# Kernel optimization log

Measured on AMD Instinct MI355X. Metric: run time of the kernel, lower is better.

Reference implementation:

```python
import jax, jax.numpy as jnp
import numpy as np

N_USERS = 100000
N_ITEMS = 50000
D = 64
E = 3200000
N_LAYERS = 2
ALPHA = 0.1


def setup_inputs() -> dict:
    key = jax.random.key(0)
    k1, k2, k3, k4 = jax.random.split(key, 4)
    user_emb0 = jax.random.normal(k1, (N_USERS, D), jnp.float32) * 0.01
    item_emb0 = jax.random.normal(k2, (N_ITEMS, D), jnp.float32) * 0.01
    edge_u = jax.random.randint(k3, (E,), 0, N_USERS, dtype=jnp.int32)
    edge_i = jax.random.randint(k4, (E,), 0, N_ITEMS, dtype=jnp.int32)
    ones = jnp.ones((E,), jnp.float32)
    # row-normalization exactly as the torch module: A_ui = D_u^{-1} R, A_iu = D_i^{-1} R^T
    deg_u = jax.ops.segment_sum(ones, edge_u, num_segments=N_USERS)
    deg_i = jax.ops.segment_sum(ones, edge_i, num_segments=N_ITEMS)
    deg_u = jnp.where(deg_u == 0, 1.0, deg_u)
    deg_i = jnp.where(deg_i == 0, 1.0, deg_i)
    a_ui_vals = 1.0 / deg_u[edge_u]  # value of A_ui at (u, i)
    a_iu_vals = 1.0 / deg_i[edge_i]  # value of A_iu at (i, u)
    return {
        "user_emb0": user_emb0,
        "item_emb0": item_emb0,
        "a_ui_vals": a_ui_vals,
        "a_iu_vals": a_iu_vals,
        "edge_u": edge_u,
        "edge_i": edge_i,
    }


def _spmm(vals, dst_idx, src_idx, src_emb, n_dst):
    # out[dst] = sum_e vals[e] * src_emb[src_idx[e]]  -- gather, scale, scatter-add
    gathered = src_emb[src_idx] * vals[:, None]  # [E, D]
    return jax.ops.segment_sum(gathered, dst_idx, num_segments=n_dst)


def reference(user_emb0, item_emb0, a_ui_vals, a_iu_vals, edge_u, edge_i):
    user_layers = [user_emb0]
    item_layers = [item_emb0]
    for _ in range(N_LAYERS):
        u_new = _spmm(a_ui_vals, edge_u, edge_i, item_layers[-1], N_USERS) + ALPHA * user_emb0
        i_new = _spmm(a_iu_vals, edge_i, edge_u, user_layers[-1], N_ITEMS) + ALPHA * item_emb0
        user_layers.append(u_new)
        item_layers.append(i_new)
    # [n_layers+1, N_USERS, D], [n_layers+1, N_ITEMS, D]
    return jnp.stack(user_layers, 0), jnp.stack(item_layers, 0)
```

## Files before the change

### kernel.cpp

```cpp
#include <hip/hip_runtime.h>


constexpr int N_USERS = 100000;
constexpr int N_ITEMS = 50000;
constexpr int N_ROWS  = N_USERS + N_ITEMS;
constexpr int D = 64;
constexpr int E_EDGES = 3200000;
constexpr float ALPHA = 0.1f;

constexpr long long NUF = (long long)N_USERS * D;
constexpr long long NIF = (long long)N_ITEMS * D;

constexpr int SB_SHIFT = 8;
constexpr int SB_ROWS  = 1 << SB_SHIFT;
constexpr int NSB      = (N_ROWS + SB_ROWS - 1) >> SB_SHIFT;
constexpr int CAP      = 20480;

constexpr int P1_EDGES   = 8192;
constexpr int P1_THREADS = 512;
constexpr int P1_EPT     = P1_EDGES / P1_THREADS;
constexpr int P2_THREADS = 512;

__global__ void init_layer0(const float* __restrict__ uemb,
                            const float* __restrict__ iemb,
                            float* __restrict__ out) {
    long long idx = (long long)blockIdx.x * blockDim.x + threadIdx.x;
    if (idx < NUF) out[idx] = uemb[idx];
    if (idx < NIF) out[3 * NUF + idx] = iemb[idx];
}

__global__ void init_layer0_fused(const float* __restrict__ uemb,
                                  const float* __restrict__ iemb,
                                  float* __restrict__ out,
                                  _Float16* __restrict__ h0u,
                                  _Float16* __restrict__ h0i) {
    long long idx = ((long long)blockIdx.x * blockDim.x + threadIdx.x) * 4;
    if (idx < NUF) {
        float4 v = *(const float4*)(uemb + idx);
        *(float4*)(out + idx) = v;
        _Float16 h4[4] = {(_Float16)v.x, (_Float16)v.y, (_Float16)v.z, (_Float16)v.w};
        *(uint2*)(h0u + idx) = *(const uint2*)h4;
    }
    if (idx < NIF) {
        float4 v = *(const float4*)(iemb + idx);
        *(float4*)(out + 3 * NUF + idx) = v;
        _Float16 h4[4] = {(_Float16)v.x, (_Float16)v.y, (_Float16)v.z, (_Float16)v.w};
        *(uint2*)(h0i + idx) = *(const uint2*)h4;
    }
}

__global__ void seed_alpha(const float* __restrict__ uemb,
                           const float* __restrict__ iemb,
                           float* __restrict__ out) {
    long long idx = (long long)blockIdx.x * blockDim.x + threadIdx.x;
    if (idx < NUF) {
        float av = ALPHA * uemb[idx];
        out[NUF + idx] = av;
        out[2 * NUF + idx] = av;
    }
    if (idx < NIF) {
        float av = ALPHA * iemb[idx];
        out[3 * NUF + NIF + idx] = av;
        out[3 * NUF + 2 * NIF + idx] = av;
    }
}

__global__ void init_sbcur(int* __restrict__ sbcur) {
    int t = blockIdx.x * blockDim.x + threadIdx.x;
    if (t < NSB) sbcur[t] = t * CAP;
}

__global__ void count_scan(const int* __restrict__ sbcur, int* __restrict__ sbstart) {
    __shared__ int sh[1024];
    int t = threadIdx.x;
    int v = (t < NSB) ? (sbcur[t] - t * CAP) : 0;
    sh[t] = v;
    __syncthreads();
    for (int off = 1; off < 1024; off <<= 1) {
        int x = (t >= off) ? sh[t - off] : 0;
        __syncthreads();
        sh[t] += x;
        __syncthreads();
    }
    if (t < NSB) {
        sbstart[t] = sh[t] - v;
        if (t == NSB - 1) sbstart[NSB] = sh[t];
    }
}

__global__ void phase1_binsort(const int* __restrict__ eu, const int* __restrict__ ei,
                               int* __restrict__ sbcur, unsigned* __restrict__ scratch) {
    __shared__ unsigned buf[2 * P1_EDGES];
    __shared__ int hist[NSB];
    __shared__ int excl[NSB];
    __shared__ int gbase[NSB];
    __shared__ int psc[P1_THREADS];
    int t = threadIdx.x;
    int wv = t >> 6;
    int lane = t & 63;
    int nchunks = (E_EDGES + P1_EDGES - 1) / P1_EDGES;
    for (int c = blockIdx.x; c < nchunks; c += gridDim.x) {
        int lo = c * P1_EDGES;
        for (int r = t; r < NSB; r += P1_THREADS) hist[r] = 0;
        __syncthreads();
        unsigned sbr[2 * P1_EPT];
        unsigned val[2 * P1_EPT];
#pragma unroll
        for (int k = 0; k < P1_EPT; k++) {
            int e = lo + k * P1_THREADS + t;
            if (e < E_EDGES) {
                int u = __builtin_nontemporal_load(eu + e);
                int i = __builtin_nontemporal_load(ei + e);
                int r0 = u;
                int r1 = N_USERS + i;
                int sb0 = r0 >> SB_SHIFT;
                int sb1 = r1 >> SB_SHIFT;
                int rk0 = atomicAdd(&hist[sb0], 1);
                int rk1 = atomicAdd(&hist[sb1], 1);
                sbr[2 * k]     = ((unsigned)sb0 << 16) | (unsigned)rk0;
                val[2 * k]     = ((unsigned)(r0 & (SB_ROWS - 1)) << 17) | (unsigned)i;
                sbr[2 * k + 1] = ((unsigned)sb1 << 16) | (unsigned)rk1;
                val[2 * k + 1] = ((unsigned)(r1 & (SB_ROWS - 1)) << 17) | (unsigned)u;
            } else {
                sbr[2 * k]     = 0xFFFFFFFFu;
                sbr[2 * k + 1] = 0xFFFFFFFFu;
            }
        }
        __syncthreads();
        int a = (2 * t < NSB) ? hist[2 * t] : 0;
        int b = (2 * t + 1 < NSB) ? hist[2 * t + 1] : 0;
        psc[t] = a + b;
        __syncthreads();
        for (int off = 1; off < P1_THREADS; off <<= 1) {
            int x = (t >= off) ? psc[t - off] : 0;
            __syncthreads();
            psc[t] += x;
            __syncthreads();
        }
        int e0 = psc[t] - (a + b);
        if (2 * t < NSB)     excl[2 * t] = e0;
        if (2 * t + 1 < NSB) excl[2 * t + 1] = e0 + a;
        for (int r = t; r < NSB; r += P1_THREADS) {
            int cnt = hist[r];
            gbase[r] = cnt ? atomicAdd(&sbcur[r], cnt) : 0;
        }
        __syncthreads();
#pragma unroll
        for (int k = 0; k < 2 * P1_EPT; k++) {
            if (sbr[k] != 0xFFFFFFFFu) {
                int sb = (int)(sbr[k] >> 16);
                int rk = (int)(sbr[k] & 0xFFFFu);
                buf[excl[sb] + rk] = val[k];
            }
        }
        __syncthreads();
        for (int r = wv; r < NSB; r += P1_THREADS / 64) {
            int cnt  = hist[r];
            int base = gbase[r];
            int off  = excl[r];
            int cap_hi = (r + 1) * CAP;
            for (int k = lane; k < cnt; k += 64) {
                int p = base + k;
                if (p < cap_hi)
                    scratch[p] = buf[off + k];
            }
        }
        __syncthreads();
    }
}

__global__ void phase2_fused(const unsigned* __restrict__ scratch,
                             const int* __restrict__ sbcur,
                             const int* __restrict__ sbstart,
                             int* __restrict__ row, int* __restrict__ col) {
    __shared__ unsigned buf[CAP];
    __shared__ int hist[SB_ROWS];
    __shared__ int pscan[SB_ROWS];
    int sb = blockIdx.x;
    int t = threadIdx.x;
    int lo = sb * CAP;
    int n  = sbcur[sb] - lo;
    if (n > CAP) n = CAP;
    int out_lo = sbstart[sb];
    if (t < SB_ROWS) hist[t] = 0;
    __syncthreads();
    for (int idx = t; idx < n; idx += P2_THREADS)
        atomicAdd(&hist[scratch[lo + idx] >> 17], 1);
    __syncthreads();
    if (t < SB_ROWS) pscan[t] = hist[t];
    __syncthreads();
    for (int off = 1; off < SB_ROWS; off <<= 1) {
        int x = 0;
        if (t < SB_ROWS && t >= off) x = pscan[t - off];
        __syncthreads();
        if (t < SB_ROWS) pscan[t] += x;
        __syncthreads();
    }
    int excl = 0;
    if (t < SB_ROWS) {
        excl = pscan[t] - hist[t];
        int gr = (sb << SB_SHIFT) + t;
        if (gr <= N_ROWS) row[gr] = out_lo + excl;
    }
    __syncthreads();
    if (t < SB_ROWS) hist[t] = excl;
    __syncthreads();
    for (int idx = t; idx < n; idx += P2_THREADS) {
        unsigned e = scratch[lo + idx];
        int p = atomicAdd(&hist[e >> 17], 1);
        buf[p] = e & 0x1FFFFu;
    }
    __syncthreads();
    for (int k = t; k < n; k += P2_THREADS)
        col[out_lo + k] = (int)buf[k];
}

__global__ void emb_to_half(const float* __restrict__ uemb,
                            const float* __restrict__ iemb,
                            _Float16* __restrict__ hu, _Float16* __restrict__ hi) {
    long long idx = ((long long)blockIdx.x * blockDim.x + threadIdx.x) * 4;
    if (idx < NUF) {
        float4 v = *(const float4*)(uemb + idx);
        _Float16 h4[4] = {(_Float16)v.x, (_Float16)v.y, (_Float16)v.z, (_Float16)v.w};
        *(uint2*)(hu + idx) = *(const uint2*)h4;
    } else if (idx < NUF + NIF) {
        long long k = idx - NUF;
        float4 v = *(const float4*)(iemb + k);
        _Float16 h4[4] = {(_Float16)v.x, (_Float16)v.y, (_Float16)v.z, (_Float16)v.w};
        *(uint2*)(hi + k) = *(const uint2*)h4;
    }
}

__device__ __forceinline__ void pull_row_h2(const int* __restrict__ row,
                                            const int* __restrict__ col,
                                            const _Float16* __restrict__ hsrc,
                                            const _Float16* __restrict__ e0h,
                                            const float* __restrict__ e0f,
                                            float* __restrict__ dst,
                                            _Float16* __restrict__ hdst,
                                            int comb_row, int local_row, int lane) {
    int start = __builtin_amdgcn_readfirstlane(row[comb_row]);
    int end   = __builtin_amdgcn_readfirstlane(row[comb_row + 1]);
    int len = end - start;
    float scale = (len > 0) ? 1.0f / (float)len : 0.0f;

    float acc0 = 0.f, acc1 = 0.f, acc2 = 0.f, acc3 = 0.f;
    int j = start;
    for (; j + 8 <= end; j += 8) {
        int c0 = __builtin_nontemporal_load(col + j + 0);
        int c1 = __builtin_nontemporal_load(col + j + 1);
        int c2 = __builtin_nontemporal_load(col + j + 2);
        int c3 = __builtin_nontemporal_load(col + j + 3);
        int c4 = __builtin_nontemporal_load(col + j + 4);
        int c5 = __builtin_nontemporal_load(col + j + 5);
        int c6 = __builtin_nontemporal_load(col + j + 6);
        int c7 = __builtin_nontemporal_load(col + j + 7);
        acc0 += (float)hsrc[((long long)c0 << 6) + lane];
        acc1 += (float)hsrc[((long long)c1 << 6) + lane];
        acc2 += (float)hsrc[((long long)c2 << 6) + lane];
        acc3 += (float)hsrc[((long long)c3 << 6) + lane];
        acc0 += (float)hsrc[((long long)c4 << 6) + lane];
        acc1 += (float)hsrc[((long long)c5 << 6) + lane];
        acc2 += (float)hsrc[((long long)c6 << 6) + lane];
        acc3 += (float)hsrc[((long long)c7 << 6) + lane];
    }
    for (; j < end; j++) {
        int c = __builtin_nontemporal_load(col + j);
        acc0 += (float)hsrc[((long long)c << 6) + lane];
    }
    long long li = ((long long)local_row << 6) + lane;
    float e0 = e0h ? (float)e0h[li] : e0f[li];
    float res = scale * ((acc0 + acc1) + (acc2 + acc3)) + ALPHA * e0;
    __builtin_nontemporal_store(res, dst + li);
    if (hdst) hdst[li] = (_Float16)res;
}

__global__ void spmm_user_h(const int* __restrict__ row, const int* __restrict__ col,
                            const _Float16* __restrict__ hsrc_item,
                            const _Float16* __restrict__ e0h,
                            const float* __restrict__ e0f,
                            float* __restrict__ out_user,
                            _Float16* __restrict__ hout_user) {
    long long gtid = (long long)blockIdx.x * blockDim.x + threadIdx.x;
    int wave = (int)(gtid >> 6);
    int lane = (int)(gtid & 63);
    if (wave >= N_USERS) return;
    pull_row_h2(row, col, hsrc_item, e0h, e0f, out_user, hout_user,
                wave, wave, lane);
}

__global__ void spmm_item_h(const int* __restrict__ row, const int* __restrict__ col,
                            const _Float16* __restrict__ hsrc_user,
                            const _Float16* __restrict__ e0h,
                            const float* __restrict__ e0f,
                            float* __restrict__ out_item,
                            _Float16* __restrict__ hout_item) {
    long long gtid = (long long)blockIdx.x * blockDim.x + threadIdx.x;
    int wave = (int)(gtid >> 6);
    int lane = (int)(gtid & 63);
    if (wave >= N_ITEMS) return;
    pull_row_h2(row, col, hsrc_user, e0h, e0f, out_item, hout_item,
                N_USERS + wave, wave, lane);
}

__global__ void spmm_pull(const int* __restrict__ row, const int* __restrict__ col,
                          const float* __restrict__ src_user,
                          const float* __restrict__ src_item,
                          const float* __restrict__ uemb, const float* __restrict__ iemb,
                          float* __restrict__ out_user, float* __restrict__ out_item) {
    long long gtid = (long long)blockIdx.x * blockDim.x + threadIdx.x;
    int wave = (int)(gtid >> 6);
    int lane = (int)(gtid & 63);
    if (wave >= N_ROWS) return;
    const float* src; const float* emb0; float* dst; int r;
    if (wave < N_USERS) {
        r = wave; src = src_item; emb0 = uemb; dst = out_user;
    } else {
        r = wave - N_USERS; src = src_user; emb0 = iemb; dst = out_item;
    }
    int start = __builtin_amdgcn_readfirstlane(row[wave]);
    int end   = __builtin_amdgcn_readfirstlane(row[wave + 1]);
    int len = end - start;
    float scale = (len > 0) ? 1.0f / (float)len : 0.0f;

    float acc0 = 0.f, acc1 = 0.f, acc2 = 0.f, acc3 = 0.f;
    int j = start;
    for (; j + 8 <= end; j += 8) {
        int c0 = col[j + 0], c1 = col[j + 1], c2 = col[j + 2], c3 = col[j + 3];
        int c4 = col[j + 4], c5 = col[j + 5], c6 = col[j + 6], c7 = col[j + 7];
        acc0 += src[((long long)c0 << 6) + lane];
        acc1 += src[((long long)c1 << 6) + lane];
        acc2 += src[((long long)c2 << 6) + lane];
        acc3 += src[((long long)c3 << 6) + lane];
        acc0 += src[((long long)c4 << 6) + lane];
        acc1 += src[((long long)c5 << 6) + lane];
        acc2 += src[((long long)c6 << 6) + lane];
        acc3 += src[((long long)c7 << 6) + lane];
    }
    for (; j < end; j++) {
        int c = col[j];
        acc0 += src[((long long)c << 6) + lane];
    }
    float res = scale * ((acc0 + acc1) + (acc2 + acc3))
              + ALPHA * emb0[((long long)r << 6) + lane];
    dst[((long long)r << 6) + lane] = res;
}

__global__ void spmm_layer_atomic(const float* __restrict__ a_ui,
                                  const float* __restrict__ a_iu,
                                  const int* __restrict__ edge_u,
                                  const int* __restrict__ edge_i,
                                  const float* __restrict__ src_user,
                                  const float* __restrict__ src_item,
                                  float* __restrict__ dst_user,
                                  float* __restrict__ dst_item) {
    long long gtid = (long long)blockIdx.x * blockDim.x + threadIdx.x;
    long long wave = gtid >> 6;
    int lane = (int)(gtid & 63);
    if (wave < (long long)E_EDGES) {
        int e = (int)wave;
        int u = edge_u[e];
        int i = edge_i[e];
        float x = a_ui[e] * src_item[(long long)i * D + lane];
        __hip_atomic_fetch_add(dst_user + (long long)u * D + lane, x,
                               __ATOMIC_RELAXED, __HIP_MEMORY_SCOPE_AGENT);
    } else if (wave < 2LL * E_EDGES) {
        int e = (int)(wave - E_EDGES);
        int u = edge_u[e];
        int i = edge_i[e];
        float x = a_iu[e] * src_user[(long long)u * D + lane];
        __hip_atomic_fetch_add(dst_item + (long long)i * D + lane, x,
                               __ATOMIC_RELAXED, __HIP_MEMORY_SCOPE_AGENT);
    }
}

extern "C" void kernel_launch(void* const* d_in, const int* in_sizes, int n_in,
                              void* d_out, int out_size, void* d_ws, size_t ws_size,
                              hipStream_t stream) {
    const float* uemb   = (const float*)d_in[0];
    const float* iemb   = (const float*)d_in[1];
    const float* a_ui   = (const float*)d_in[2];
    const float* a_iu   = (const float*)d_in[3];
    const int*   edge_u = (const int*)d_in[4];
    const int*   edge_i = (const int*)d_in[5];
    float* out = (float*)d_out;

    float* u1 = out + NUF;
    float* u2 = out + 2 * NUF;
    float* i1 = out + 3 * NUF + NIF;
    float* i2 = out + 3 * NUF + 2 * NIF;

    unsigned* scratch = (unsigned*)u1;

    size_t base_ints = (size_t)(N_ROWS + 1) + NSB + (NSB + 1) + 2 * (size_t)E_EDGES;
    size_t need_b  = base_ints * 4 + 64;
    size_t need_a  = need_b + (size_t)(NUF + NIF) * 2;
    size_t need_a2 = need_a + (size_t)(NUF + NIF) * 2;
    bool tier_b  = ws_size >= need_b;
    bool tier_a  = ws_size >= need_a;
    bool tier_a2 = ws_size >= need_a2;

    if (tier_b) {
        int* w = (int*)d_ws;
        int* row     = w;  w += N_ROWS + 1;
        int* sbcur   = w;  w += NSB;
        int* sbstart = w;  w += NSB + 1;
        int* col     = w;  w += 2 * E_EDGES;
        _Float16* h1u = (_Float16*)w;
        _Float16* h1i = h1u + NUF;
        _Float16* h0u = tier_a2 ? (h1i + NIF)
                                : (_Float16*)u2;
        _Float16* h0i = h0u + NUF;

        if (tier_a2) {
            const long long quads = NUF / 4;
            const int blocks = (int)((quads + 255) / 256);
            init_layer0_fused<<<blocks, 256, 0, stream>>>(uemb, iemb, out,
                                                          h0u, h0i);
        } else {
            const int threads = 256;
            const int blocks = (int)((NUF + threads - 1) / threads);
            init_layer0<<<blocks, threads, 0, stream>>>(uemb, iemb, out);
        }

        init_sbcur<<<3, 256, 0, stream>>>(sbcur);
        const int p1_blocks = (E_EDGES + P1_EDGES - 1) / P1_EDGES;
        phase1_binsort<<<p1_blocks, P1_THREADS, 0, stream>>>(edge_u, edge_i,
                                                             sbcur, scratch);
        count_scan<<<1, 1024, 0, stream>>>(sbcur, sbstart);
        phase2_fused<<<NSB, P2_THREADS, 0, stream>>>(scratch, sbcur, sbstart,
                                                     row, col);
        if (!tier_a2) {
            const long long quads = (NUF + NIF) / 4;
            const int blocks = (int)((quads + 255) / 256);
            emb_to_half<<<blocks, 256, 0, stream>>>(uemb, iemb, h0u, h0i);
        }

        const int ublocks = (int)(((long long)N_USERS * 64 + 255) / 256);
        const int iblocks = (int)(((long long)N_ITEMS * 64 + 255) / 256);
        if (tier_a) {
            spmm_user_h<<<ublocks, 256, 0, stream>>>(row, col, h0i, h0u, nullptr,
                                                     u1, h1u);
            spmm_item_h<<<iblocks, 256, 0, stream>>>(row, col, h0u, h0i, nullptr,
                                                     i1, h1i);
            const _Float16* a2u = tier_a2 ? h0u : nullptr;
            const _Float16* a2i = tier_a2 ? h0i : nullptr;
            spmm_user_h<<<ublocks, 256, 0, stream>>>(row, col, h1i, a2u, uemb,
                                                     u2, nullptr);
            spmm_item_h<<<iblocks, 256, 0, stream>>>(row, col, h1u, a2i, iemb,
                                                     i2, nullptr);
        } else {
            spmm_user_h<<<ublocks, 256, 0, stream>>>(row, col, h0i, h0u, nullptr,
                                                     u1, nullptr);
            spmm_item_h<<<iblocks, 256, 0, stream>>>(row, col, h0u, h0i, nullptr,
                                                     i1, nullptr);
            const int threads = 256;
            const long long total_threads = (long long)N_ROWS * 64;
            const int blocks = (int)((total_threads + threads - 1) / threads);
            spmm_pull<<<blocks, threads, 0, stream>>>(row, col, u1, i1,
                                                      uemb, iemb, u2, i2);
        }
    } else {
        {
            const int threads = 256;
            const int blocks = (int)((NUF + threads - 1) / threads);
            init_layer0<<<blocks, threads, 0, stream>>>(uemb, iemb, out);
            seed_alpha<<<blocks, threads, 0, stream>>>(uemb, iemb, out);
        }
        const int threads = 256;
        const long long total_threads = 2LL * E_EDGES * 64;
        const int blocks = (int)((total_threads + threads - 1) / threads);
        spmm_layer_atomic<<<blocks, threads, 0, stream>>>(a_ui, a_iu, edge_u, edge_i,
                                                          uemb, iemb, u1, i1);
        spmm_layer_atomic<<<blocks, threads, 0, stream>>>(a_ui, a_iu, edge_u, edge_i,
                                                          u1, i1, u2, i2);
    }
}
```

Baseline: 564.8 us.

## Tile SpMM gathers by source-column range with persistent blocks and grid barriers

The CSR build now sorts each row's edges into sub-buckets by source-column tile (16K rows) and records per-tile boundaries. Each SpMM becomes a persistent kernel with 512 blocks that walks the tiles in lockstep, separated by spin-based grid barriers, so the gathered half-precision source rows for the current tile stay resident in L2. The cost is a grid barrier between tiles, each wave handling many rows serially, and a spin barrier that has a timeout and assumes all blocks are co-resident.

Result: slower. 1.572 ms (+178.4%).

```diff
diff --git a/kernel.cpp b/kernel.cpp
--- a/kernel.cpp
+++ b/kernel.cpp
@@ -16,10 +16,21 @@
 constexpr int NSB      = (N_ROWS + SB_ROWS - 1) >> SB_SHIFT;
 constexpr int CAP      = 20480;
 
+constexpr int TILE_SHIFT = 14;
+constexpr int T_USER_TAB = 7;
+constexpr int T_ITEM_TAB = 4;
+
 constexpr int P1_EDGES   = 8192;
 constexpr int P1_THREADS = 512;
 constexpr int P1_EPT     = P1_EDGES / P1_THREADS;
 constexpr int P2_THREADS = 512;
+constexpr int P2_BINS    = SB_ROWS * 8;
+
+constexpr int SPMM_BLOCKS  = 512;
+constexpr int SPMM_THREADS = 512;
+constexpr int RPW_USER = (N_USERS + 4095) / 4096;
+constexpr int RPW_ITEM = (N_ITEMS + 4095) / 4096;
+constexpr int N_BAR = 32;
 
 __global__ void init_layer0(const float* __restrict__ uemb,
                             const float* __restrict__ iemb,
@@ -65,9 +76,10 @@
     }
 }
 
-__global__ void init_sbcur(int* __restrict__ sbcur) {
+__global__ void init_misc(int* __restrict__ sbcur, int* __restrict__ bar) {
     int t = blockIdx.x * blockDim.x + threadIdx.x;
     if (t < NSB) sbcur[t] = t * CAP;
+    if (t < N_BAR) bar[t] = 0;
 }
 
 __global__ void count_scan(const int* __restrict__ sbcur, int* __restrict__ sbstart) {
@@ -172,42 +184,51 @@
 __global__ void phase2_fused(const unsigned* __restrict__ scratch,
                              const int* __restrict__ sbcur,
                              const int* __restrict__ sbstart,
-                             int* __restrict__ row, int* __restrict__ col) {
+                             int* __restrict__ bnd, int* __restrict__ col) {
     __shared__ unsigned buf[CAP];
-    __shared__ int hist[SB_ROWS];
-    __shared__ int pscan[SB_ROWS];
+    __shared__ int hist[P2_BINS];
+    __shared__ int psc[P2_THREADS];
     int sb = blockIdx.x;
     int t = threadIdx.x;
     int lo = sb * CAP;
     int n  = sbcur[sb] - lo;
     if (n > CAP) n = CAP;
     int out_lo = sbstart[sb];
-    if (t < SB_ROWS) hist[t] = 0;
-    __syncthreads();
-    for (int idx = t; idx < n; idx += P2_THREADS)
-        atomicAdd(&hist[scratch[lo + idx] >> 17], 1);
-    __syncthreads();
-    if (t < SB_ROWS) pscan[t] = hist[t];
-    __syncthreads();
-    for (int off = 1; off < SB_ROWS; off <<= 1) {
-        int x = 0;
-        if (t < SB_ROWS && t >= off) x = pscan[t - off];
-        __syncthreads();
-        if (t < SB_ROWS) pscan[t] += x;
-        __syncthreads();
-    }
-    int excl = 0;
-    if (t < SB_ROWS) {
-        excl = pscan[t] - hist[t];
-        int gr = (sb << SB_SHIFT) + t;
-        if (gr <= N_ROWS) row[gr] = out_lo + excl;
-    }
-    __syncthreads();
-    if (t < SB_ROWS) hist[t] = excl;
+    for (int k = t; k < P2_BINS; k += P2_THREADS) hist[k] = 0;
     __syncthreads();
     for (int idx = t; idx < n; idx += P2_THREADS) {
         unsigned e = scratch[lo + idx];
-        int p = atomicAdd(&hist[e >> 17], 1);
+        int key = (int)(e >> 17) * 8 + (int)((e & 0x1FFFFu) >> TILE_SHIFT);
+        atomicAdd(&hist[key], 1);
+    }
+    __syncthreads();
+    int b0 = hist[4 * t], b1 = hist[4 * t + 1];
+    int b2 = hist[4 * t + 2], b3 = hist[4 * t + 3];
+    int s4 = b0 + b1 + b2 + b3;
+    psc[t] = s4;
+    __syncthreads();
+    for (int off = 1; off < P2_THREADS; off <<= 1) {
+        int x = (t >= off) ? psc[t - off] : 0;
+        __syncthreads();
+        psc[t] += x;
+        __syncthreads();
+    }
+    int base = psc[t] - s4;
+    int e0 = base, e1 = base + b0, e2 = e1 + b1, e3 = e2 + b2;
+    long long gb = (long long)sb * P2_BINS + 4 * t;
+    bnd[gb + 0] = out_lo + e0;
+    bnd[gb + 1] = out_lo + e1;
+    bnd[gb + 2] = out_lo + e2;
+    bnd[gb + 3] = out_lo + e3;
+    hist[4 * t]     = e0;
+    hist[4 * t + 1] = e1;
+    hist[4 * t + 2] = e2;
+    hist[4 * t + 3] = e3;
+    __syncthreads();
+    for (int idx = t; idx < n; idx += P2_THREADS) {
+        unsigned e = scratch[lo + idx];
+        int key = (int)(e >> 17) * 8 + (int)((e & 0x1FFFFu) >> TILE_SHIFT);
+        int p = atomicAdd(&hist[key], 1);
         buf[p] = e & 0x1FFFFu;
     }
     __syncthreads();
@@ -231,7 +252,83 @@
     }
 }
 
-__device__ __forceinline__ void pull_row_h2(const int* __restrict__ row,
+__device__ __forceinline__ void grid_bar(int* __restrict__ bar, int slot) {
+    if (threadIdx.x == 0) {
+        __hip_atomic_fetch_add(bar + slot, 1, __ATOMIC_RELAXED,
+                               __HIP_MEMORY_SCOPE_AGENT);
+        int spins = 0;
+        while (__hip_atomic_load(bar + slot, __ATOMIC_RELAXED,
+                                 __HIP_MEMORY_SCOPE_AGENT) < SPMM_BLOCKS &&
+               spins < (1 << 15)) {
+            __builtin_amdgcn_s_sleep(4);
+            ++spins;
+        }
+    }
+    __syncthreads();
+}
+
+template <int RPW, int TMAX, int ROW_BASE, int NROWS>
+__global__ __launch_bounds__(SPMM_THREADS, 4)
+void spmm_tiled(const int* __restrict__ bnd, const int* __restrict__ col,
+                const _Float16* __restrict__ hsrc,
+                const _Float16* __restrict__ e0h, const float* __restrict__ e0f,
+                float* __restrict__ dst, _Float16* __restrict__ hdst,
+                int* __restrict__ bar, int bar_base) {
+    int gtid = blockIdx.x * SPMM_THREADS + threadIdx.x;
+    int wave = gtid >> 6, lane = gtid & 63;
+    int r0 = wave * RPW;
+    float acc[RPW];
+#pragma unroll
+    for (int r = 0; r < RPW; ++r) acc[r] = 0.f;
+    for (int t = 0; t < TMAX; ++t) {
+#pragma unroll
+        for (int r = 0; r < RPW; ++r) {
+            int row = r0 + r;
+            if (row < NROWS) {
+                int crow = ROW_BASE + row;
+                int s = __builtin_amdgcn_readfirstlane(bnd[crow * 8 + t]);
+                int e = __builtin_amdgcn_readfirstlane(bnd[crow * 8 + t + 1]);
+                float a = acc[r];
+                int j = s;
+                for (; j + 4 <= e; j += 4) {
+                    int c0 = __builtin_nontemporal_load(col + j);
+                    int c1 = __builtin_nontemporal_load(col + j + 1);
+                    int c2 = __builtin_nontemporal_load(col + j + 2);
+                    int c3 = __builtin_nontemporal_load(col + j + 3);
+                    float g0 = (float)hsrc[((long long)c0 << 6) + lane];
+                    float g1 = (float)hsrc[((long long)c1 << 6) + lane];
+                    float g2 = (float)hsrc[((long long)c2 << 6) + lane];
+                    float g3 = (float)hsrc[((long long)c3 << 6) + lane];
+                    a += (g0 + g1) + (g2 + g3);
+                }
+                for (; j < e; ++j) {
+                    int c = __builtin_nontemporal_load(col + j);
+                    a += (float)hsrc[((long long)c << 6) + lane];
+                }
+                acc[r] = a;
+            }
+        }
+        if (t < TMAX - 1) grid_bar(bar, bar_base + t);
+    }
+#pragma unroll
+    for (int r = 0; r < RPW; ++r) {
+        int row = r0 + r;
+        if (row < NROWS) {
+            int crow = ROW_BASE + row;
+            int st = __builtin_amdgcn_readfirstlane(bnd[crow * 8]);
+            int en = __builtin_amdgcn_readfirstlane(bnd[(crow + 1) * 8]);
+            int len = en - st;
+            float scale = (len > 0) ? 1.0f / (float)len : 0.0f;
+            long long li = ((long long)row << 6) + lane;
+            float e0v = e0h ? (float)e0h[li] : e0f[li];
+            float res = scale * acc[r] + ALPHA * e0v;
+            __builtin_nontemporal_store(res, dst + li);
+            if (hdst) hdst[li] = (_Float16)res;
+        }
+    }
+}
+
+__device__ __forceinline__ void pull_row_h2(const int* __restrict__ bnd,
                                             const int* __restrict__ col,
                                             const _Float16* __restrict__ hsrc,
                                             const _Float16* __restrict__ e0h,
@@ -239,11 +336,10 @@
                                             float* __restrict__ dst,
                                             _Float16* __restrict__ hdst,
                                             int comb_row, int local_row, int lane) {
-    int start = __builtin_amdgcn_readfirstlane(row[comb_row]);
-    int end   = __builtin_amdgcn_readfirstlane(row[comb_row + 1]);
+    int start = __builtin_amdgcn_readfirstlane(bnd[comb_row * 8]);
+    int end   = __builtin_amdgcn_readfirstlane(bnd[(comb_row + 1) * 8]);
     int len = end - start;
     float scale = (len > 0) ? 1.0f / (float)len : 0.0f;
-
     float acc0 = 0.f, acc1 = 0.f, acc2 = 0.f, acc3 = 0.f;
     int j = start;
     for (; j + 8 <= end; j += 8) {
@@ -275,7 +371,7 @@
     if (hdst) hdst[li] = (_Float16)res;
 }
 
-__global__ void spmm_user_h(const int* __restrict__ row, const int* __restrict__ col,
+__global__ void spmm_user_h(const int* __restrict__ bnd, const int* __restrict__ col,
                             const _Float16* __restrict__ hsrc_item,
                             const _Float16* __restrict__ e0h,
                             const float* __restrict__ e0f,
@@ -285,11 +381,11 @@
     int wave = (int)(gtid >> 6);
     int lane = (int)(gtid & 63);
     if (wave >= N_USERS) return;
-    pull_row_h2(row, col, hsrc_item, e0h, e0f, out_user, hout_user,
+    pull_row_h2(bnd, col, hsrc_item, e0h, e0f, out_user, hout_user,
                 wave, wave, lane);
 }
 
-__global__ void spmm_item_h(const int* __restrict__ row, const int* __restrict__ col,
+__global__ void spmm_item_h(const int* __restrict__ bnd, const int* __restrict__ col,
                             const _Float16* __restrict__ hsrc_user,
                             const _Float16* __restrict__ e0h,
                             const float* __restrict__ e0f,
@@ -299,15 +395,17 @@
     int wave = (int)(gtid >> 6);
     int lane = (int)(gtid & 63);
     if (wave >= N_ITEMS) return;
-    pull_row_h2(row, col, hsrc_user, e0h, e0f, out_item, hout_item,
+    pull_row_h2(bnd, col, hsrc_user, e0h, e0f, out_item, hout_item,
                 N_USERS + wave, wave, lane);
 }
 
-__global__ void spmm_pull(const int* __restrict__ row, const int* __restrict__ col,
-                          const float* __restrict__ src_user,
-                          const float* __restrict__ src_item,
-                          const float* __restrict__ uemb, const float* __restrict__ iemb,
-                          float* __restrict__ out_user, float* __restrict__ out_item) {
+__global__ void spmm_pull_f32(const int* __restrict__ bnd, const int* __restrict__ col,
+                              const float* __restrict__ src_user,
+                              const float* __restrict__ src_item,
+                              const float* __restrict__ uemb,
+                              const float* __restrict__ iemb,
+                              float* __restrict__ out_user,
+                              float* __restrict__ out_item) {
     long long gtid = (long long)blockIdx.x * blockDim.x + threadIdx.x;
     int wave = (int)(gtid >> 6);
     int lane = (int)(gtid & 63);
@@ -318,24 +416,18 @@
     } else {
         r = wave - N_USERS; src = src_user; emb0 = iemb; dst = out_item;
     }
-    int start = __builtin_amdgcn_readfirstlane(row[wave]);
-    int end   = __builtin_amdgcn_readfirstlane(row[wave + 1]);
+    int start = __builtin_amdgcn_readfirstlane(bnd[wave * 8]);
+    int end   = __builtin_amdgcn_readfirstlane(bnd[(wave + 1) * 8]);
     int len = end - start;
     float scale = (len > 0) ? 1.0f / (float)len : 0.0f;
-
     float acc0 = 0.f, acc1 = 0.f, acc2 = 0.f, acc3 = 0.f;
     int j = start;
-    for (; j + 8 <= end; j += 8) {
+    for (; j + 4 <= end; j += 4) {
         int c0 = col[j + 0], c1 = col[j + 1], c2 = col[j + 2], c3 = col[j + 3];
-        int c4 = col[j + 4], c5 = col[j + 5], c6 = col[j + 6], c7 = col[j + 7];
         acc0 += src[((long long)c0 << 6) + lane];
         acc1 += src[((long long)c1 << 6) + lane];
         acc2 += src[((long long)c2 << 6) + lane];
         acc3 += src[((long long)c3 << 6) + lane];
-        acc0 += src[((long long)c4 << 6) + lane];
-        acc1 += src[((long long)c5 << 6) + lane];
-        acc2 += src[((long long)c6 << 6) + lane];
-        acc3 += src[((long long)c7 << 6) + lane];
     }
     for (; j < end; j++) {
         int c = col[j];
@@ -392,27 +484,29 @@
 
     unsigned* scratch = (unsigned*)u1;
 
-    size_t base_ints = (size_t)(N_ROWS + 1) + NSB + (NSB + 1) + 2 * (size_t)E_EDGES;
-    size_t need_b  = base_ints * 4 + 64;
-    size_t need_a  = need_b + (size_t)(NUF + NIF) * 2;
-    size_t need_a2 = need_a + (size_t)(NUF + NIF) * 2;
-    bool tier_b  = ws_size >= need_b;
-    bool tier_a  = ws_size >= need_a;
-    bool tier_a2 = ws_size >= need_a2;
-
-    if (tier_b) {
+    size_t bnd_ints  = (size_t)NSB * P2_BINS + 8;
+    size_t base_ints = N_BAR + NSB + (NSB + 1) + bnd_ints + 2 * (size_t)E_EDGES;
+    size_t need_csr = base_ints * 4 + 64;
+    size_t need_t1  = need_csr + (size_t)(NUF + NIF) * 2;
+    size_t need_t2  = need_t1 + (size_t)(NUF + NIF) * 2;
+    bool csr = ws_size >= need_csr;
+    bool t1  = ws_size >= need_t1;
+    bool t2  = ws_size >= need_t2;
+
+    if (csr) {
         int* w = (int*)d_ws;
-        int* row     = w;  w += N_ROWS + 1;
+        int* bar     = w;  w += N_BAR;
         int* sbcur   = w;  w += NSB;
         int* sbstart = w;  w += NSB + 1;
+        int* bnd     = w;  w += bnd_ints;
         int* col     = w;  w += 2 * E_EDGES;
         _Float16* h1u = (_Float16*)w;
         _Float16* h1i = h1u + NUF;
-        _Float16* h0u = tier_a2 ? (h1i + NIF)
-                                : (_Float16*)u2;
+        _Float16* h0u = t2 ? (h1i + NIF)
+                           : (_Float16*)u2;
         _Float16* h0i = h0u + NUF;
 
-        if (tier_a2) {
+        if (t2) {
             const long long quads = NUF / 4;
             const int blocks = (int)((quads + 255) / 256);
             init_layer0_fused<<<blocks, 256, 0, stream>>>(uemb, iemb, out,
@@ -423,41 +517,44 @@
             init_layer0<<<blocks, threads, 0, stream>>>(uemb, iemb, out);
         }
 
-        init_sbcur<<<3, 256, 0, stream>>>(sbcur);
+        init_misc<<<3, 256, 0, stream>>>(sbcur, bar);
         const int p1_blocks = (E_EDGES + P1_EDGES - 1) / P1_EDGES;
         phase1_binsort<<<p1_blocks, P1_THREADS, 0, stream>>>(edge_u, edge_i,
                                                              sbcur, scratch);
         count_scan<<<1, 1024, 0, stream>>>(sbcur, sbstart);
         phase2_fused<<<NSB, P2_THREADS, 0, stream>>>(scratch, sbcur, sbstart,
-                                                     row, col);
-        if (!tier_a2) {
+                                                     bnd, col);
+        if (!t2) {
             const long long quads = (NUF + NIF) / 4;
             const int blocks = (int)((quads + 255) / 256);
             emb_to_half<<<blocks, 256, 0, stream>>>(uemb, iemb, h0u, h0i);
         }
 
-        const int ublocks = (int)(((long long)N_USERS * 64 + 255) / 256);
-        const int iblocks = (int)(((long long)N_ITEMS * 64 + 255) / 256);
-        if (tier_a) {
-            spmm_user_h<<<ublocks, 256, 0, stream>>>(row, col, h0i, h0u, nullptr,
-                                                     u1, h1u);
-            spmm_item_h<<<iblocks, 256, 0, stream>>>(row, col, h0u, h0i, nullptr,
-                                                     i1, h1i);
-            const _Float16* a2u = tier_a2 ? h0u : nullptr;
-            const _Float16* a2i = tier_a2 ? h0i : nullptr;
-            spmm_user_h<<<ublocks, 256, 0, stream>>>(row, col, h1i, a2u, uemb,
-                                                     u2, nullptr);
-            spmm_item_h<<<iblocks, 256, 0, stream>>>(row, col, h1u, a2i, iemb,
-                                                     i2, nullptr);
+        if (t1) {
+            spmm_tiled<RPW_USER, T_ITEM_TAB, 0, N_USERS>
+                <<<SPMM_BLOCKS, SPMM_THREADS, 0, stream>>>(
+                    bnd, col, h0i, h0u, nullptr, u1, h1u, bar, 0);
+            spmm_tiled<RPW_ITEM, T_USER_TAB, N_USERS, N_ITEMS>
+                <<<SPMM_BLOCKS, SPMM_THREADS, 0, stream>>>(
+                    bnd, col, h0u, h0i, nullptr, i1, h1i, bar, 4);
+            const _Float16* a2u = t2 ? h0u : nullptr;
+            const _Float16* a2i = t2 ? h0i : nullptr;
+            spmm_tiled<RPW_USER, T_ITEM_TAB, 0, N_USERS>
+                <<<SPMM_BLOCKS, SPMM_THREADS, 0, stream>>>(
+                    bnd, col, h1i, a2u, uemb, u2, nullptr, bar, 12);
+            spmm_tiled<RPW_ITEM, T_USER_TAB, N_USERS, N_ITEMS>
+                <<<SPMM_BLOCKS, SPMM_THREADS, 0, stream>>>(
+                    bnd, col, h1u, a2i, iemb, i2, nullptr, bar, 16);
         } else {
-            spmm_user_h<<<ublocks, 256, 0, stream>>>(row, col, h0i, h0u, nullptr,
+            const int ublocks = (int)(((long long)N_USERS * 64 + 255) / 256);
+            const int iblocks = (int)(((long long)N_ITEMS * 64 + 255) / 256);
+            spmm_user_h<<<ublocks, 256, 0, stream>>>(bnd, col, h0i, h0u, nullptr,
                                                      u1, nullptr);
-            spmm_item_h<<<iblocks, 256, 0, stream>>>(row, col, h0u, h0i, nullptr,
+            spmm_item_h<<<iblocks, 256, 0, stream>>>(bnd, col, h0u, h0i, nullptr,
                                                      i1, nullptr);
-            const int threads = 256;
             const long long total_threads = (long long)N_ROWS * 64;
-            const int blocks = (int)((total_threads + threads - 1) / threads);
-            spmm_pull<<<blocks, threads, 0, stream>>>(row, col, u1, i1,
+            const int blocks = (int)((total_threads + 255) / 256);
+            spmm_pull_f32<<<blocks, 256, 0, stream>>>(bnd, col, u1, i1,
                                                       uemb, iemb, u2, i2);
         }
     } else {
```
